# Kernel optimization log

Measured on AMD Instinct MI355X. Metric: run time of the kernel, lower is better.

The kernel has to match this reference:

```python
import jax, jax.numpy as jnp
import numpy as np

STATE_DIM = 256
MAX_NODES = 64
EPS = 1e-5
EDGE_THRESHOLD = 0.3


def _glorot(key, shape):
    fan_in = shape[0]
    bound = 1.0 / np.sqrt(fan_in)
    return jax.random.uniform(key, shape, jnp.float32, -bound, bound)


def setup_inputs() -> dict:
    key = jax.random.key(0)
    ks = jax.random.split(key, 16)
    D = STATE_DIM
    d2, d4 = D // 2, D // 4
    inp = {
        "state_sequence": jax.random.normal(ks[0], (256, 128, D), jnp.float32),
        # node encoder
        "W1": _glorot(ks[1], (D, d2)), "b1": jnp.zeros((d2,), jnp.float32),
        "W2": _glorot(ks[2], (d2, d4)), "b2": jnp.zeros((d4,), jnp.float32),
        "gamma": jnp.ones((d4,), jnp.float32), "beta": jnp.zeros((d4,), jnp.float32),
        # edge predictor (input dim d2 = 2*d4)
        "E1": _glorot(ks[3], (d2, 64)), "bE1": jnp.zeros((64,), jnp.float32),
        "E2": _glorot(ks[4], (64, 32)), "bE2": jnp.zeros((32,), jnp.float32),
        "E3": _glorot(ks[5], (32, 1)), "bE3": jnp.zeros((1,), jnp.float32),
        # strength estimator
        "S1": _glorot(ks[6], (d2, 32)), "bS1": jnp.zeros((32,), jnp.float32),
        "S2": _glorot(ks[7], (32, 1)), "bS2": jnp.zeros((1,), jnp.float32),
    }
    return inp


def reference(state_sequence, W1, b1, W2, b2, gamma, beta,
              E1, bE1, E2, bE2, E3, bE3, S1, bS1, S2, bS2):
    B, S, D = state_sequence.shape
    N = MAX_NODES
    # pad if seq shorter than max_nodes (static shapes, here S >= N so no-op branch)
    if S < N:
        state_sequence = jnp.pad(state_sequence, ((0, 0), (0, N - S), (0, 0)))
        S = N
    # linspace indices, truncated to long like torch.linspace(..., dtype=long)
    idx = jnp.linspace(0.0, S - 1, N).astype(jnp.int32)
    nodes = state_sequence[:, idx]                      # [B, N, D]

    # node encoder: Linear -> ReLU -> (Dropout eval) -> Linear -> LayerNorm
    h = jax.nn.relu(jnp.einsum('bnd,de->bne', nodes, W1) + b1)
    h = jnp.einsum('bnd,de->bne', h, W2) + b2           # [B, N, D//4]
    mu = jnp.mean(h, axis=-1, keepdims=True)
    var = jnp.mean((h - mu) ** 2, axis=-1, keepdims=True)
    node_features = (h - mu) * jax.lax.rsqrt(var + EPS) * gamma + beta
    node_features = jnp.nan_to_num(node_features, nan=0.0)

    d4 = node_features.shape[-1]
    # pair input is concat([f_i, f_j]); split first-layer weights to avoid
    # materializing the [B,N,N,2*d4] concat tensor.
    # edge predictor first layer
    ei = jnp.einsum('bnd,dh->bnh', node_features, E1[:d4])   # [B, N, 64]
    ej = jnp.einsum('bnd,dh->bnh', node_features, E1[d4:])
    he = jax.nn.relu(ei[:, :, None, :] + ej[:, None, :, :] + bE1)  # [B,N,N,64]
    he = jax.nn.relu(jnp.einsum('bijh,hk->bijk', he, E2) + bE2)    # [B,N,N,32]
    edge_prob = jax.nn.sigmoid(jnp.einsum('bijk,ko->bijo', he, E3) + bE3)[..., 0]

    # strength estimator
    si = jnp.einsum('bnd,dh->bnh', node_features, S1[:d4])
    sj = jnp.einsum('bnd,dh->bnh', node_features, S1[d4:])
    hs = jax.nn.relu(si[:, :, None, :] + sj[:, None, :, :] + bS1)  # [B,N,N,32]
    strength = jnp.tanh(jnp.einsum('bijk,ko->bijo', hs, S2) + bS2)[..., 0]

    offdiag = 1.0 - jnp.eye(N, dtype=edge_prob.dtype)   # i != j only
    adjacency = edge_prob * offdiag
    strengths = strength * offdiag
    adjacency = jnp.where(adjacency > EDGE_THRESHOLD, adjacency, 0.0)
    return node_features, adjacency, strengths
```

## Files before the change

### kernel.cpp

```cpp
#include <hip/hip_runtime.h>
#include <hip/hip_bf16.h>
#include <math.h>

typedef __attribute__((ext_vector_type(8))) short short8;
typedef __attribute__((ext_vector_type(4))) short short4v;
typedef __attribute__((ext_vector_type(4))) float f32x4;
typedef __attribute__((ext_vector_type(2))) _Float16 h2;
typedef __attribute__((ext_vector_type(8))) _Float16 h8;

__device__ __forceinline__ short f2bf(float f) {
    __hip_bfloat16 h = __float2bfloat16(f);
    return __builtin_bit_cast(short, h);
}

__global__ __launch_bounds__(256)
void kernelA0(const float* __restrict__ W1, const float* __restrict__ W2,
              const float* __restrict__ E1, const float* __restrict__ S1,
              short* __restrict__ wT)
{
    const int tid = blockIdx.x * 256 + threadIdx.x;
    {   const int k = tid >> 7, n = tid & 127;
        wT[n * 256 + k] = f2bf(W1[tid]); }
    if (tid < 8192) {
        const int k = tid >> 6, n = tid & 63;
        wT[32768 + n * 128 + k] = f2bf(W2[tid]); }
    if (tid < 8192) {
        const int rr = tid >> 6, c = tid & 63;
        const int o = (rr < 64) ? c : (64 + c);
        const int k = (rr < 64) ? rr : (rr - 64);
        wT[40960 + o * 64 + k] = f2bf(E1[tid]); }
    if (tid < 4096) {
        const int rr = tid >> 5, c = tid & 31;
        const int o = (rr < 64) ? (128 + c) : (160 + c);
        const int k = (rr < 64) ? rr : (rr - 64);
        wT[40960 + o * 64 + k] = f2bf(S1[tid]); }
}

constexpr int XS_S  = 264;
constexpr int H1B_S = 136;
constexpr int HS_S  = 68;
constexpr int NNF_S = 72;
constexpr int EJW   = 72;
constexpr int SJW   = 40;

constexpr int OFF_XS  = 0;
constexpr int OFF_EIH = 0;
constexpr int OFF_EJH = 9216;
constexpr int OFF_SIH = 18432;
constexpr int OFF_SJH = 23552;
constexpr int OFF_H1B = 33792;
constexpr int OFF_HS  = 51200;
constexpr int LDS_BYTES = 68608;

__global__ __launch_bounds__(1024)
void kernelF(const float* __restrict__ x,
             const float* __restrict__ b1, const float* __restrict__ b2,
             const float* __restrict__ gamma, const float* __restrict__ beta,
             const short* __restrict__ wT,
             const float* __restrict__ bE1, const float* __restrict__ E2,
             const float* __restrict__ bE2, const float* __restrict__ E3,
             const float* __restrict__ bE3, const float* __restrict__ bS1,
             const float* __restrict__ S2, const float* __restrict__ bS2,
             float* __restrict__ out_nf, float* __restrict__ out_adj,
             float* __restrict__ out_str)
{
    extern __shared__ char lds[];
    short*    XsS  = (short*)(lds + OFF_XS);
    short*    h1BS = (short*)(lds + OFF_H1B);
    float*    HsS  = (float*)(lds + OFF_HS);
    short*    nfBS = (short*)(lds + OFF_H1B);
    _Float16* eihS = (_Float16*)(lds + OFF_EIH);
    _Float16* ejhS = (_Float16*)(lds + OFF_EJH);
    _Float16* sihS = (_Float16*)(lds + OFF_SIH);
    _Float16* sjhS = (_Float16*)(lds + OFF_SJH);
    __shared__ float bE2s[32], E3s[32];
    __shared__ _Float16 s2hS[32];

    const int t = threadIdx.x, b = blockIdx.x;
    const int w = t >> 6, l = t & 63, g = l >> 4, r = l & 15;
    const short* W1T = wT;
    const short* W2T = wT + 32768;
    const short* WcT = wT + 40960;

    if (t < 32)       bE2s[t] = bE2[t];
    else if (t < 64)  E3s[t - 32] = E3[t - 32];
    else if (t < 96)  s2hS[t - 64] = (_Float16)S2[t - 64];

    h8 aE00, aE10, aE01, aE11;
#pragma unroll
    for (int e = 0; e < 8; ++e) {
        aE00[e] = (_Float16)E2[(size_t)(8 * g + e) * 32 + r];
        aE10[e] = (_Float16)E2[(size_t)(8 * g + e + 32) * 32 + r];
        aE01[e] = (_Float16)E2[(size_t)(8 * g + e) * 32 + r + 16];
        aE11[e] = (_Float16)E2[(size_t)(8 * g + e + 32) * 32 + r + 16];
    }
    const float bE3v = bE3[0], bS2v = bS2[0];
    const h8 z8 = {(_Float16)0.f, (_Float16)0.f, (_Float16)0.f, (_Float16)0.f,
                   (_Float16)0.f, (_Float16)0.f, (_Float16)0.f, (_Float16)0.f};

    {
        const int row = t >> 4, c0 = t & 15;
        const int srow = (row == 63) ? 127 : (int)((float)row * (127.0f / 63.0f));
        const float* xrow = x + ((size_t)b * 128 + srow) * 256;
#pragma unroll
        for (int i = 0; i < 4; ++i) {
            const int c4 = (c0 + 16 * i) * 4;
            const float4 v = *(const float4*)(xrow + c4);
            short4v sv;
            sv[0] = f2bf(v.x); sv[1] = f2bf(v.y); sv[2] = f2bf(v.z); sv[3] = f2bf(v.w);
            *(short4v*)&XsS[row * XS_S + c4] = sv;
        }
    }
    __syncthreads();

    {
        const int mt = w >> 2, nb = (w & 3) << 1;
        const int aRow = (16 * mt + r) * XS_S;
#pragma unroll
        for (int np = 0; np < 2; ++np) {
            const int n = ((nb + np) << 4) + r;
            f32x4 acca = {0.f, 0.f, 0.f, 0.f};
            f32x4 accb = {0.f, 0.f, 0.f, 0.f};
#pragma unroll
            for (int ks = 0; ks < 4; ++ks) {
                const short8 a0  = *(const short8*)&XsS[aRow + 32 * ks + 8 * g];
                const short8 a1  = *(const short8*)&XsS[aRow + 32 * (ks + 4) + 8 * g];
                const short8 bwa = *(const short8*)(W1T + (size_t)n * 256 + 32 * ks + 8 * g);
                const short8 bwb = *(const short8*)(W1T + (size_t)n * 256 + 32 * (ks + 4) + 8 * g);
                acca = __builtin_amdgcn_mfma_f32_16x16x32_bf16(a0, bwa, acca, 0, 0, 0);
                accb = __builtin_amdgcn_mfma_f32_16x16x32_bf16(a1, bwb, accb, 0, 0, 0);
            }
            const float b1v = b1[n];
#pragma unroll
            for (int q = 0; q < 4; ++q)
                h1BS[(16 * mt + 4 * g + q) * H1B_S + n] = f2bf(fmaxf(acca[q] + accb[q] + b1v, 0.f));
        }
    }
    __syncthreads();

    {
        const int mt = w >> 2;
        const int n = ((w & 3) << 4) + r;
        const int aRow = (16 * mt + r) * H1B_S;
        f32x4 acca = {0.f, 0.f, 0.f, 0.f};
        f32x4 accb = {0.f, 0.f, 0.f, 0.f};
#pragma unroll
        for (int ks2 = 0; ks2 < 2; ++ks2) {
            const short8 ha0 = *(const short8*)&h1BS[aRow + 32 * (2 * ks2) + 8 * g];
            const short8 ha1 = *(const short8*)&h1BS[aRow + 32 * (2 * ks2 + 1) + 8 * g];
            const short8 bw0 = *(const short8*)(W2T + (size_t)n * 128 + 32 * (2 * ks2) + 8 * g);
            const short8 bw1 = *(const short8*)(W2T + (size_t)n * 128 + 32 * (2 * ks2 + 1) + 8 * g);
            acca = __builtin_amdgcn_mfma_f32_16x16x32_bf16(ha0, bw0, acca, 0, 0, 0);
            accb = __builtin_amdgcn_mfma_f32_16x16x32_bf16(ha1, bw1, accb, 0, 0, 0);
        }
        const float b2v = b2[n];
#pragma unroll
        for (int q = 0; q < 4; ++q)
            HsS[(16 * mt + 4 * g + q) * HS_S + n] = acca[q] + accb[q] + b2v;
    }
    __syncthreads();

    {
        const int row = t >> 4, c4 = (t & 15) * 4;
        const float4 v = *(const float4*)&HsS[row * HS_S + c4];
        float s = v.x + v.y + v.z + v.w;
        s += __shfl_xor(s, 1); s += __shfl_xor(s, 2);
        s += __shfl_xor(s, 4); s += __shfl_xor(s, 8);
        const float mu = s * (1.0f / 64.0f);
        float vs = 0.f;
        { const float d0 = v.x-mu, d1 = v.y-mu, d2 = v.z-mu, d3 = v.w-mu;
          vs = fmaf(d0,d0, fmaf(d1,d1, fmaf(d2,d2, d3*d3))); }
        vs += __shfl_xor(vs, 1); vs += __shfl_xor(vs, 2);
        vs += __shfl_xor(vs, 4); vs += __shfl_xor(vs, 8);
        const float rstd = rsqrtf(vs * (1.0f / 64.0f) + 1e-5f);
        const float4 gv = *(const float4*)(gamma + c4);
        const float4 bv = *(const float4*)(beta  + c4);
        float4 o;
        o.x = fmaf((v.x - mu) * rstd, gv.x, bv.x);
        o.y = fmaf((v.y - mu) * rstd, gv.y, bv.y);
        o.z = fmaf((v.z - mu) * rstd, gv.z, bv.z);
        o.w = fmaf((v.w - mu) * rstd, gv.w, bv.w);
        *(float4*)(out_nf + (size_t)b * 4096 + (size_t)row * 64 + c4) = o;
        short4v ob;
        ob[0] = f2bf(o.x); ob[1] = f2bf(o.y); ob[2] = f2bf(o.z); ob[3] = f2bf(o.w);
        *(short4v*)&nfBS[row * NNF_S + c4] = ob;
    }
    __syncthreads();

    {
        const int mt = w >> 2;
        const short8 na0 = *(const short8*)&nfBS[(16 * mt + r) * NNF_S + 8 * g];
        const short8 na1 = *(const short8*)&nfBS[(16 * mt + r) * NNF_S + 32 + 8 * g];
#pragma unroll
        for (int k3 = 0; k3 < 3; ++k3) {
            const int ot = (w & 3) * 3 + k3;
            const int c = 16 * ot + r;
            const short8 bw0 = *(const short8*)(WcT + (size_t)c * 64 + 8 * g);
            const short8 bw1 = *(const short8*)(WcT + (size_t)c * 64 + 32 + 8 * g);
            f32x4 acc = {0.f, 0.f, 0.f, 0.f};
            acc = __builtin_amdgcn_mfma_f32_16x16x32_bf16(na0, bw0, acc, 0, 0, 0);
            acc = __builtin_amdgcn_mfma_f32_16x16x32_bf16(na1, bw1, acc, 0, 0, 0);
            if (ot < 4) {
                const float bv = bE1[c];
#pragma unroll
                for (int q = 0; q < 4; ++q)
                    eihS[(16 * mt + 4 * g + q) * EJW + c] = (_Float16)(acc[q] + bv);
            } else if (ot < 8) {
#pragma unroll
                for (int q = 0; q < 4; ++q)
                    ejhS[(16 * mt + 4 * g + q) * EJW + (c - 64)] = (_Float16)acc[q];
            } else if (ot < 10) {
                const float bv = bS1[c - 128];
#pragma unroll
                for (int q = 0; q < 4; ++q)
                    sihS[(16 * mt + 4 * g + q) * SJW + (c - 128)] = (_Float16)(acc[q] + bv);
            } else {
#pragma unroll
                for (int q = 0; q < 4; ++q)
                    sjhS[(16 * mt + 4 * g + q) * SJW + (c - 160)] = (_Float16)acc[q];
            }
        }
    }
    __syncthreads();

    const int sj_ = t & 63;
    const int sib = (t >> 6) * 4;
    for (int jt = 0; jt < 4; ++jt) {
        const int j = (jt << 4) + r;
        const h8 ej0 = *(const h8*)&ejhS[j * EJW + 8 * g];
        const h8 ej1 = *(const h8*)&ejhS[j * EJW + 32 + 8 * g];

#pragma unroll
        for (int ii = 0; ii < 4; ++ii) {
            const int ig = 4 * w + ii;
            const h8 ei0 = *(const h8*)&eihS[ig * EJW + 8 * g];
            const h8 ei1 = *(const h8*)&eihS[ig * EJW + 32 + 8 * g];

            const h8 b0 = __builtin_elementwise_max(ei0 + ej0, z8);
            const h8 b1 = __builtin_elementwise_max(ei1 + ej1, z8);

            f32x4 acc0 = {0.f, 0.f, 0.f, 0.f};
            f32x4 acc1 = {0.f, 0.f, 0.f, 0.f};
            acc0 = __builtin_amdgcn_mfma_f32_16x16x32_f16(aE00, b0, acc0, 0, 0, 0);
            acc0 = __builtin_amdgcn_mfma_f32_16x16x32_f16(aE10, b1, acc0, 0, 0, 0);
            acc1 = __builtin_amdgcn_mfma_f32_16x16x32_f16(aE01, b0, acc1, 0, 0, 0);
            acc1 = __builtin_amdgcn_mfma_f32_16x16x32_f16(aE11, b1, acc1, 0, 0, 0);

            float pe = 0.f;
#pragma unroll
            for (int q = 0; q < 4; ++q) {
                const int k0 = 4 * g + q;
                pe = fmaf(fmaxf(acc0[q] + bE2s[k0], 0.f), E3s[k0], pe);
                pe = fmaf(fmaxf(acc1[q] + bE2s[k0 + 16], 0.f), E3s[k0 + 16], pe);
            }
            pe += __shfl_xor(pe, 16);
            pe += __shfl_xor(pe, 32);

            if (l < 16) {
                const float z = pe + bE3v;
                const float p = 1.0f / (1.0f + __expf(-z));
                const float av = (j == ig || !(p > 0.3f)) ? 0.f : p;
                out_adj[(size_t)b * 4096 + (size_t)ig * 64 + j] = av;
            }
        }

        {
            const int ig = sib + jt;
            float sacc = 0.f;
#pragma unroll
            for (int c = 0; c < 4; ++c) {
                const h8 si8 = *(const h8*)&sihS[ig * SJW + 8 * c];
                const h8 sj8 = *(const h8*)&sjhS[sj_ * SJW + 8 * c];
                const h8 s2  = *(const h8*)&s2hS[8 * c];
                const h8 hs = __builtin_elementwise_max(si8 + sj8, z8);
                const h2 p0 = __builtin_shufflevector(hs, hs, 0, 1);
                const h2 p1 = __builtin_shufflevector(hs, hs, 2, 3);
                const h2 p2 = __builtin_shufflevector(hs, hs, 4, 5);
                const h2 p3 = __builtin_shufflevector(hs, hs, 6, 7);
                const h2 q0 = __builtin_shufflevector(s2, s2, 0, 1);
                const h2 q1 = __builtin_shufflevector(s2, s2, 2, 3);
                const h2 q2 = __builtin_shufflevector(s2, s2, 4, 5);
                const h2 q3 = __builtin_shufflevector(s2, s2, 6, 7);
                sacc = __builtin_amdgcn_fdot2(p0, q0, sacc, false);
                sacc = __builtin_amdgcn_fdot2(p1, q1, sacc, false);
                sacc = __builtin_amdgcn_fdot2(p2, q2, sacc, false);
                sacc = __builtin_amdgcn_fdot2(p3, q3, sacc, false);
            }
            const float xs = sacc + bS2v;
            const float e2x = __expf(2.0f * xs);
            const float sv = (sj_ == ig) ? 0.f : (e2x - 1.0f) / (e2x + 1.0f);
            out_str[(size_t)b * 4096 + (size_t)ig * 64 + sj_] = sv;
        }
    }
}

extern "C" void kernel_launch(void* const* d_in, const int* in_sizes, int n_in,
                              void* d_out, int out_size, void* d_ws, size_t ws_size,
                              hipStream_t stream)
{
    const float* x     = (const float*)d_in[0];
    const float* W1    = (const float*)d_in[1];
    const float* b1    = (const float*)d_in[2];
    const float* W2    = (const float*)d_in[3];
    const float* b2    = (const float*)d_in[4];
    const float* gamma = (const float*)d_in[5];
    const float* beta  = (const float*)d_in[6];
    const float* E1    = (const float*)d_in[7];
    const float* bE1   = (const float*)d_in[8];
    const float* E2    = (const float*)d_in[9];
    const float* bE2   = (const float*)d_in[10];
    const float* E3    = (const float*)d_in[11];
    const float* bE3   = (const float*)d_in[12];
    const float* S1    = (const float*)d_in[13];
    const float* bS1   = (const float*)d_in[14];
    const float* S2    = (const float*)d_in[15];
    const float* bS2   = (const float*)d_in[16];

    float* out     = (float*)d_out;
    float* out_nf  = out;
    float* out_adj = out + 1048576;
    float* out_str = out + 2097152;

    short* wT = (short*)d_ws;

    (void)hipFuncSetAttribute((const void*)kernelF,
        hipFuncAttributeMaxDynamicSharedMemorySize, LDS_BYTES);

    kernelA0<<<128, 256, 0, stream>>>(W1, W2, E1, S1, wT);

    kernelF<<<256, 1024, LDS_BYTES, stream>>>(
        x, b1, b2, gamma, beta, wT,
        bE1, E2, bE2, E3, bE3, bS1, S2, bS2,
        out_nf, out_adj, out_str);
}
```

Before: 39.40 us.

## Split each batch's pair computation across two blocks, recomputing node encoder

The fused kernel now launches a 2x256 grid, and each block handles half of the i rows of the pairwise edge and strength stages for one batch. Both blocks redundantly recompute the node encoder, LayerNorm and first-layer projections, and only block zero writes node features. This doubles the number of blocks to improve occupancy across CUs, at the cost of duplicated encoder GEMM work and input loads.

After: 54.22 us. +37.6%, slower.

```diff
diff --git a/kernel.cpp b/kernel.cpp
--- a/kernel.cpp
+++ b/kernel.cpp
@@ -76,7 +76,9 @@
     __shared__ float bE2s[32], E3s[32];
     __shared__ _Float16 s2hS[32];
 
-    const int t = threadIdx.x, b = blockIdx.x;
+    const int t = threadIdx.x;
+    const int s = blockIdx.x;
+    const int b = blockIdx.y;
     const int w = t >> 6, l = t & 63, g = l >> 4, r = l & 15;
     const short* W1T = wT;
     const short* W2T = wT + 32768;
@@ -163,10 +165,10 @@
     {
         const int row = t >> 4, c4 = (t & 15) * 4;
         const float4 v = *(const float4*)&HsS[row * HS_S + c4];
-        float s = v.x + v.y + v.z + v.w;
-        s += __shfl_xor(s, 1); s += __shfl_xor(s, 2);
-        s += __shfl_xor(s, 4); s += __shfl_xor(s, 8);
-        const float mu = s * (1.0f / 64.0f);
+        float sm = v.x + v.y + v.z + v.w;
+        sm += __shfl_xor(sm, 1); sm += __shfl_xor(sm, 2);
+        sm += __shfl_xor(sm, 4); sm += __shfl_xor(sm, 8);
+        const float mu = sm * (1.0f / 64.0f);
         float vs = 0.f;
         { const float d0 = v.x-mu, d1 = v.y-mu, d2 = v.z-mu, d3 = v.w-mu;
           vs = fmaf(d0,d0, fmaf(d1,d1, fmaf(d2,d2, d3*d3))); }
@@ -180,7 +182,8 @@
         o.y = fmaf((v.y - mu) * rstd, gv.y, bv.y);
         o.z = fmaf((v.z - mu) * rstd, gv.z, bv.z);
         o.w = fmaf((v.w - mu) * rstd, gv.w, bv.w);
-        *(float4*)(out_nf + (size_t)b * 4096 + (size_t)row * 64 + c4) = o;
+        if (s == 0)
+            *(float4*)(out_nf + (size_t)b * 4096 + (size_t)row * 64 + c4) = o;
         short4v ob;
         ob[0] = f2bf(o.x); ob[1] = f2bf(o.y); ob[2] = f2bf(o.z); ob[3] = f2bf(o.w);
         *(short4v*)&nfBS[row * NNF_S + c4] = ob;
@@ -223,16 +226,14 @@
     }
     __syncthreads();
 
-    const int sj_ = t & 63;
-    const int sib = (t >> 6) * 4;
     for (int jt = 0; jt < 4; ++jt) {
         const int j = (jt << 4) + r;
         const h8 ej0 = *(const h8*)&ejhS[j * EJW + 8 * g];
         const h8 ej1 = *(const h8*)&ejhS[j * EJW + 32 + 8 * g];
 
 #pragma unroll
-        for (int ii = 0; ii < 4; ++ii) {
-            const int ig = 4 * w + ii;
+        for (int ii = 0; ii < 2; ++ii) {
+            const int ig = 32 * s + 2 * w + ii;
             const h8 ei0 = *(const h8*)&eihS[ig * EJW + 8 * g];
             const h8 ei1 = *(const h8*)&eihS[ig * EJW + 32 + 8 * g];
 
@@ -263,14 +264,19 @@
                 out_adj[(size_t)b * 4096 + (size_t)ig * 64 + j] = av;
             }
         }
-
-        {
-            const int ig = sib + jt;
+    }
+
+    {
+        const int j = t & 63;
+        const int ib = 32 * s + (t >> 6) * 2;
+#pragma unroll
+        for (int ii = 0; ii < 2; ++ii) {
+            const int ig = ib + ii;
             float sacc = 0.f;
 #pragma unroll
             for (int c = 0; c < 4; ++c) {
                 const h8 si8 = *(const h8*)&sihS[ig * SJW + 8 * c];
-                const h8 sj8 = *(const h8*)&sjhS[sj_ * SJW + 8 * c];
+                const h8 sj8 = *(const h8*)&sjhS[j * SJW + 8 * c];
                 const h8 s2  = *(const h8*)&s2hS[8 * c];
                 const h8 hs = __builtin_elementwise_max(si8 + sj8, z8);
                 const h2 p0 = __builtin_shufflevector(hs, hs, 0, 1);
@@ -288,8 +294,8 @@
             }
             const float xs = sacc + bS2v;
             const float e2x = __expf(2.0f * xs);
-            const float sv = (sj_ == ig) ? 0.f : (e2x - 1.0f) / (e2x + 1.0f);
-            out_str[(size_t)b * 4096 + (size_t)ig * 64 + sj_] = sv;
+            const float sv = (j == ig) ? 0.f : (e2x - 1.0f) / (e2x + 1.0f);
+            out_str[(size_t)b * 4096 + (size_t)ig * 64 + j] = sv;
         }
     }
 }
@@ -328,7 +334,7 @@
 
     kernelA0<<<128, 256, 0, stream>>>(W1, W2, E1, S1, wT);
 
-    kernelF<<<256, 1024, LDS_BYTES, stream>>>(
+    kernelF<<<dim3(2, 256), 1024, LDS_BYTES, stream>>>(
         x, b1, b2, gamma, beta, wT,
         bE1, E2, bE2, E3, bE3, bS1, S2, bS2,
         out_nf, out_adj, out_str);
```
